# Kernel optimization log

Measured on AMD Instinct MI355X. Metric: run time of the kernel, lower is better.

Reference implementation:

```python
import jax, jax.numpy as jnp
import numpy as np


def _gcn_norm(edge_index, num_nodes, dtype):
    # PyG GCNConv.norm: add self-loops (weight 1), symmetric deg^{-1/2} normalization
    row, col = edge_index[0], edge_index[1]
    loop = jnp.arange(num_nodes, dtype=row.dtype)
    row = jnp.concatenate([row, loop])
    col = jnp.concatenate([col, loop])
    ew = jnp.ones(row.shape[0], dtype=dtype)
    deg = jax.ops.segment_sum(ew, row, num_segments=num_nodes)
    dis = jnp.where(deg > 0, jax.lax.rsqrt(deg), 0.0)
    norm = dis[row] * ew * dis[col]
    return row, col, norm


def _masked_gcn_conv(x, row, col, norm, sigma, W, b, num_nodes):
    # mask_features: edge gather -> diff/sigma -> square -> scatter-add -> exp mask
    h = (x[col] - x[row]) / sigma            # [E, F]
    h = norm[:, None] * h * h                # [E, F]
    mask = jax.ops.segment_sum(h, row, num_segments=num_nodes)        # [N, F]
    deg = jax.ops.segment_sum(jnp.ones_like(norm), row, num_segments=num_nodes)  # degree(source), >=1 due to self-loops
    x = x * jnp.exp(-mask / deg[:, None])
    # GCNConv: linear transform then normalized aggregation source->target
    xw = x @ W                               # [N, O]
    out = jax.ops.segment_sum(norm[:, None] * xw[row], col, num_segments=num_nodes)
    return out + b


def setup_inputs() -> dict:
    key = jax.random.key(0)
    ks = jax.random.split(key, 8)
    N, E, F, H, C = 100000, 1600000, 128, 64, 40
    g = 1.414  # xavier gain used for sigma
    return {
        "x": jax.random.normal(ks[0], (N, F), jnp.float32),
        "edge_index": jax.random.randint(ks[1], (2, E), 0, N, jnp.int64),
        "sigma1": jax.random.uniform(ks[2], (1, F), jnp.float32, -1.0, 1.0) * (g * np.sqrt(6.0 / (1 + F))),
        "W1": jax.random.normal(ks[3], (F, H), jnp.float32) * (1.0 / np.sqrt(F)),
        "b1": jnp.zeros((H,), jnp.float32),
        "sigma2": jax.random.uniform(ks[4], (1, H), jnp.float32, -1.0, 1.0) * (g * np.sqrt(6.0 / (1 + H))),
        "W2": jax.random.normal(ks[5], (H, C), jnp.float32) * (1.0 / np.sqrt(H)),
        "b2": jnp.zeros((C,), jnp.float32),
    }


def reference(x, edge_index, sigma1, W1, b1, sigma2, W2, b2):
    N = x.shape[0]
    row, col, norm = _gcn_norm(edge_index, N, x.dtype)
    x = _masked_gcn_conv(x, row, col, norm, sigma1, W1, b1, N)
    x = jax.nn.relu(x)
    # dropout is identity in eval mode
    x = _masked_gcn_conv(x, row, col, norm, sigma2, W2, b2, N)
    return jax.nn.log_softmax(x, axis=1)
```

## Files before the change

### kernel.cpp

```cpp
#include <hip/hip_runtime.h>
#include <cmath>

constexpr int F1 = 128;
constexpr int H  = 64;
constexpr int NC = 40;
constexpr int NPART = 4;

constexpr int SCAN_TPB = 256;
constexpr int SCAN_IPT = 8;
constexpr int SCAN_EPB = SCAN_TPB * SCAN_IPT;

__device__ inline unsigned short f2bf(float f) {
    union { float f; unsigned u; } v; v.f = f;
    return (unsigned short)((v.u + 0x7FFFu + ((v.u >> 16) & 1u)) >> 16);
}
__device__ inline float bflo(unsigned p) { union { float f; unsigned u; } v; v.u = p << 16; return v.f; }
__device__ inline float bfhi(unsigned p) { union { float f; unsigned u; } v; v.u = p & 0xFFFF0000u; return v.f; }
__device__ inline void unpack8(uint4 raw, float* d) {
    d[0] = bflo(raw.x); d[1] = bfhi(raw.x); d[2] = bflo(raw.y); d[3] = bfhi(raw.y);
    d[4] = bflo(raw.z); d[5] = bfhi(raw.z); d[6] = bflo(raw.w); d[7] = bfhi(raw.w);
}

__global__ void isg_kernel(const float* __restrict__ s1, float* __restrict__ i1,
                           const float* __restrict__ s2, float* __restrict__ i2) {
    int i = threadIdx.x;
    if (i < F1) i1[i] = 1.0f / s1[i];
    if (i < H)  i2[i] = 1.0f / s2[i];
}

__global__ void count8_prep_kernel(const int* __restrict__ row, const int* __restrict__ col,
                                   int* __restrict__ cntO, int* __restrict__ cntI,
                                   int E, int chunk, int stride, int cntBlocks,
                                   const float* __restrict__ x, const float* __restrict__ isg,
                                   unsigned short* __restrict__ u, size_t n8) {
    int bid = blockIdx.x;
    if (bid < cntBlocks) {
        int p = bid & (NPART - 1);
        int gid = bid / NPART;
        unsigned lo = (unsigned)(p * chunk);
        for (int e = gid * blockDim.x + threadIdx.x; e < E; e += stride) {
            int r = row[e], c = col[e];
            if ((unsigned)r - lo < (unsigned)chunk) atomicAdd(&cntO[r], 1);
            if ((unsigned)c - lo < (unsigned)chunk) atomicAdd(&cntI[c], 1);
        }
    } else {
        size_t idx = (size_t)(bid - cntBlocks) * blockDim.x + threadIdx.x;
        if (idx >= n8) return;
        size_t base = idx * 8;
        int fk = (int)(base % (size_t)F1);
        float4 a0 = *(const float4*)&x[base];
        float4 a1 = *(const float4*)&x[base + 4];
        float4 s0 = *(const float4*)&isg[fk];
        float4 s1 = *(const float4*)&isg[fk + 4];
        uint4 p4;
        p4.x = (unsigned)f2bf(a0.x * s0.x) | ((unsigned)f2bf(a0.y * s0.y) << 16);
        p4.y = (unsigned)f2bf(a0.z * s0.z) | ((unsigned)f2bf(a0.w * s0.w) << 16);
        p4.z = (unsigned)f2bf(a1.x * s1.x) | ((unsigned)f2bf(a1.y * s1.y) << 16);
        p4.w = (unsigned)f2bf(a1.z * s1.z) | ((unsigned)f2bf(a1.w * s1.w) << 16);
        *(uint4*)&u[base] = p4;
    }
}

__global__ void scan_partial_kernel(const int* __restrict__ cnt, int* __restrict__ bsum, int M) {
    __shared__ int red[SCAN_TPB];
    int t = threadIdx.x;
    int i0 = blockIdx.x * SCAN_EPB + t * SCAN_IPT;
    int s = 0;
#pragma unroll
    for (int k = 0; k < SCAN_IPT; ++k) {
        int i = i0 + k;
        if (i < M) s += cnt[i];
    }
    red[t] = s;
    __syncthreads();
    for (int off = SCAN_TPB / 2; off > 0; off >>= 1) {
        if (t < off) red[t] += red[t + off];
        __syncthreads();
    }
    if (t == 0) bsum[blockIdx.x] = red[0];
}

__global__ void scan_offsets_kernel(int* __restrict__ bsum, int nb,
                                    int* __restrict__ rowptrO, int* __restrict__ rowptrI,
                                    int N, int E) {
    __shared__ int sh[1024];
    int t = threadIdx.x;
    sh[t] = (t < nb) ? bsum[t] : 0;
    __syncthreads();
    for (int off = 1; off < 1024; off <<= 1) {
        int v = (t >= off) ? sh[t - off] : 0;
        __syncthreads();
        sh[t] += v;
        __syncthreads();
    }
    if (t < nb) bsum[t] = (t > 0) ? sh[t - 1] : 0;
    if (t == 0) { rowptrO[N] = E; rowptrI[N] = E; }
}

__global__ void scan_final_kernel(int* __restrict__ cntO, int* __restrict__ cntI,
                                  const int* __restrict__ bsum,
                                  int* __restrict__ rowptrO, int* __restrict__ rowptrI,
                                  float* __restrict__ dis, int N, int E) {
    __shared__ int sh[SCAN_TPB];
    int t = threadIdx.x;
    int M = 2 * N;
    const int* cnt = cntO;
    int i0 = blockIdx.x * SCAN_EPB + t * SCAN_IPT;
    int cv[SCAN_IPT], pre[SCAN_IPT];
    int run = 0;
#pragma unroll
    for (int k = 0; k < SCAN_IPT; ++k) {
        int i = i0 + k;
        cv[k] = (i < M) ? cnt[i] : 0;
        pre[k] = run;
        run += cv[k];
    }
    sh[t] = run;
    __syncthreads();
    for (int off = 1; off < SCAN_TPB; off <<= 1) {
        int v = (t >= off) ? sh[t - off] : 0;
        __syncthreads();
        sh[t] += v;
        __syncthreads();
    }
    int toff = ((t > 0) ? sh[t - 1] : 0) + bsum[blockIdx.x];
#pragma unroll
    for (int k = 0; k < SCAN_IPT; ++k) {
        int i = i0 + k;
        if (i < M) {
            int val = toff + pre[k];
            if (i < N) {
                rowptrO[i] = val;
                cntO[i] = val;
                dis[i] = rsqrtf((float)(cv[k] + 1));
            } else {
                rowptrI[i - N] = val - E;
                cntI[i - N] = val - E;
            }
        }
    }
}

__global__ void build8_kernel(const int* __restrict__ row, const int* __restrict__ col,
                              int* __restrict__ curO, int* __restrict__ curI,
                              int2* __restrict__ adjO2, int2* __restrict__ adjI2,
                              const float* __restrict__ dis,
                              int E, int chunk, int stride) {
    int p = blockIdx.x & (NPART - 1);
    int gid = blockIdx.x / NPART;
    unsigned lo = (unsigned)(p * chunk);
    for (int e = gid * blockDim.x + threadIdx.x; e < E; e += stride) {
        int r = row[e], c = col[e];
        bool inR = (unsigned)r - lo < (unsigned)chunk;
        bool inC = (unsigned)c - lo < (unsigned)chunk;
        if (inR | inC) {
            float nrm = dis[r] * dis[c];
            int nb = __float_as_int(nrm);
            if (inR) adjO2[atomicAdd(&curO[r], 1)] = make_int2(c, nb);
            if (inC) adjI2[atomicAdd(&curI[c], 1)] = make_int2(r, nb);
        }
    }
}

template<int F, int O, int R>
__global__ void fused_mask_gemm_kernel(const int* __restrict__ rowptr, const int2* __restrict__ adj2,
                                       const float* __restrict__ sig,
                                       const unsigned short* __restrict__ u,
                                       const float* __restrict__ W,
                                       unsigned short* __restrict__ Ybf, int N) {
    constexpr int NT = R * 64;
    constexpr int G = F / 8;
    constexpr int NPI = 64 / G;
    __shared__ __align__(16) float Ws[F * O];
    __shared__ __align__(16) float Xs[R][F];
    int tid = threadIdx.x;
    for (int i = tid; i < F * O; i += NT) Ws[i] = W[i];
    int w = tid >> 6, lane = tid & 63;
    int h = lane / G, j = lane % G;
    int base = blockIdx.x * R;
    int r = base + w;
    if (r < N) {
        int beg = rowptr[r], end = rowptr[r + 1];
        float inv_deg = 1.0f / (float)(end - beg + 1);
        float ur[8], acc[8];
        unpack8(*(const uint4*)&u[(size_t)r * F + 8 * j], ur);
#pragma unroll
        for (int k = 0; k < 8; ++k) acc[k] = 0.0f;
        for (int t = beg; t < end; t += 2 * NPI) {
            int e0 = t + h, e1 = t + NPI + h;
            int2 a0 = adj2[min(e0, end - 1)];
            int2 a1 = adj2[min(e1, end - 1)];
            float n0 = (e0 < end) ? __int_as_float(a0.y) : 0.0f;
            float n1 = (e1 < end) ? __int_as_float(a1.y) : 0.0f;
            uint4 rw0 = *(const uint4*)&u[(size_t)a0.x * F + 8 * j];
            uint4 rw1 = *(const uint4*)&u[(size_t)a1.x * F + 8 * j];
            float uc[8];
            unpack8(rw0, uc);
#pragma unroll
            for (int q = 0; q < 8; ++q) {
                float d = uc[q] - ur[q];
                acc[q] = fmaf(n0 * d, d, acc[q]);
            }
            unpack8(rw1, uc);
#pragma unroll
            for (int q = 0; q < 8; ++q) {
                float d = uc[q] - ur[q];
                acc[q] = fmaf(n1 * d, d, acc[q]);
            }
        }
#pragma unroll
        for (int off = G; off < 64; off <<= 1) {
#pragma unroll
            for (int k = 0; k < 8; ++k) acc[k] += __shfl_xor(acc[k], off);
        }
        if (h == 0) {
            float4 s0 = *(const float4*)&sig[8 * j];
            float4 s1 = *(const float4*)&sig[8 * j + 4];
            float sg[8] = {s0.x, s0.y, s0.z, s0.w, s1.x, s1.y, s1.z, s1.w};
            float xm[8];
#pragma unroll
            for (int k = 0; k < 8; ++k) xm[k] = ur[k] * sg[k] * expf(-acc[k] * inv_deg);
            *(float4*)&Xs[w][8 * j]     = make_float4(xm[0], xm[1], xm[2], xm[3]);
            *(float4*)&Xs[w][8 * j + 4] = make_float4(xm[4], xm[5], xm[6], xm[7]);
        }
    } else if (h == 0) {
        *(float4*)&Xs[w][8 * j]     = make_float4(0.f, 0.f, 0.f, 0.f);
        *(float4*)&Xs[w][8 * j + 4] = make_float4(0.f, 0.f, 0.f, 0.f);
    }
    __syncthreads();
    if (w < 2) {
        int r0 = base + 4 * w;
        if (r0 < N && lane < O) {
            float a0 = 0.f, a1 = 0.f, a2 = 0.f, a3 = 0.f;
#pragma unroll
            for (int fq = 0; fq < F / 4; ++fq) {
                float4 x0 = *(const float4*)&Xs[4 * w + 0][4 * fq];
                float4 x1 = *(const float4*)&Xs[4 * w + 1][4 * fq];
                float4 x2 = *(const float4*)&Xs[4 * w + 2][4 * fq];
                float4 x3 = *(const float4*)&Xs[4 * w + 3][4 * fq];
                float w0 = Ws[(4 * fq + 0) * O + lane];
                float w1 = Ws[(4 * fq + 1) * O + lane];
                float w2 = Ws[(4 * fq + 2) * O + lane];
                float w3 = Ws[(4 * fq + 3) * O + lane];
                a0 = fmaf(x0.x, w0, a0); a0 = fmaf(x0.y, w1, a0); a0 = fmaf(x0.z, w2, a0); a0 = fmaf(x0.w, w3, a0);
                a1 = fmaf(x1.x, w0, a1); a1 = fmaf(x1.y, w1, a1); a1 = fmaf(x1.z, w2, a1); a1 = fmaf(x1.w, w3, a1);
                a2 = fmaf(x2.x, w0, a2); a2 = fmaf(x2.y, w1, a2); a2 = fmaf(x2.z, w2, a2); a2 = fmaf(x2.w, w3, a2);
                a3 = fmaf(x3.x, w0, a3); a3 = fmaf(x3.y, w1, a3); a3 = fmaf(x3.z, w2, a3); a3 = fmaf(x3.w, w3, a3);
            }
            float o0 = __shfl_xor(a0, 1);
            float o1 = __shfl_xor(a1, 1);
            float o2 = __shfl_xor(a2, 1);
            float o3 = __shfl_xor(a3, 1);
            if (!(lane & 1)) {
                *(unsigned*)&Ybf[(size_t)r0 * O + lane] = (unsigned)f2bf(a0) | ((unsigned)f2bf(o0) << 16);
                if (r0 + 1 < N) *(unsigned*)&Ybf[(size_t)(r0 + 1) * O + lane] = (unsigned)f2bf(a1) | ((unsigned)f2bf(o1) << 16);
                if (r0 + 2 < N) *(unsigned*)&Ybf[(size_t)(r0 + 2) * O + lane] = (unsigned)f2bf(a2) | ((unsigned)f2bf(o2) << 16);
                if (r0 + 3 < N) *(unsigned*)&Ybf[(size_t)(r0 + 3) * O + lane] = (unsigned)f2bf(a3) | ((unsigned)f2bf(o3) << 16);
            }
        }
    }
}

__global__ void agg_relu_kernel(const int* __restrict__ rowptr, const int2* __restrict__ adj2,
                                const float* __restrict__ dis, const unsigned short* __restrict__ ybf,
                                const float* __restrict__ bias,
                                unsigned short* __restrict__ u2, const float* __restrict__ isg2, int N) {
    int c = blockIdx.x * (blockDim.x >> 6) + (threadIdx.x >> 6);
    if (c >= N) return;
    int lane = threadIdx.x & 63;
    int h = lane >> 3, j = lane & 7;
    int beg = rowptr[c], end = rowptr[c + 1];
    float acc[8];
#pragma unroll
    for (int k = 0; k < 8; ++k) acc[k] = 0.0f;
    for (int t = beg; t < end; t += 16) {
        int e0 = t + h, e1 = t + 8 + h;
        int2 a0 = adj2[min(e0, end - 1)];
        int2 a1 = adj2[min(e1, end - 1)];
        float n0 = (e0 < end) ? __int_as_float(a0.y) : 0.0f;
        float n1 = (e1 < end) ? __int_as_float(a1.y) : 0.0f;
        uint4 rw0 = *(const uint4*)&ybf[(size_t)a0.x * H + 8 * j];
        uint4 rw1 = *(const uint4*)&ybf[(size_t)a1.x * H + 8 * j];
        float v[8];
        unpack8(rw0, v);
#pragma unroll
        for (int q = 0; q < 8; ++q) acc[q] = fmaf(n0, v[q], acc[q]);
        unpack8(rw1, v);
#pragma unroll
        for (int q = 0; q < 8; ++q) acc[q] = fmaf(n1, v[q], acc[q]);
    }
#pragma unroll
    for (int off = 8; off < 64; off <<= 1) {
#pragma unroll
        for (int k = 0; k < 8; ++k) acc[k] += __shfl_xor(acc[k], off);
    }
    if (h == 0) {
        float dc = dis[c];
        float sv[8];
        unpack8(*(const uint4*)&ybf[(size_t)c * H + 8 * j], sv);
        float4 b0 = *(const float4*)&bias[8 * j];
        float4 b1v = *(const float4*)&bias[8 * j + 4];
        float bb[8] = {b0.x, b0.y, b0.z, b0.w, b1v.x, b1v.y, b1v.z, b1v.w};
        float4 s0 = *(const float4*)&isg2[8 * j];
        float4 s1 = *(const float4*)&isg2[8 * j + 4];
        float sg[8] = {s0.x, s0.y, s0.z, s0.w, s1.x, s1.y, s1.z, s1.w};
        float hv[8];
        float d2 = dc * dc;
#pragma unroll
        for (int k = 0; k < 8; ++k) hv[k] = fmaxf(fmaf(d2, sv[k], acc[k]) + bb[k], 0.0f);
        uint4 p;
        p.x = (unsigned)f2bf(hv[0] * sg[0]) | ((unsigned)f2bf(hv[1] * sg[1]) << 16);
        p.y = (unsigned)f2bf(hv[2] * sg[2]) | ((unsigned)f2bf(hv[3] * sg[3]) << 16);
        p.z = (unsigned)f2bf(hv[4] * sg[4]) | ((unsigned)f2bf(hv[5] * sg[5]) << 16);
        p.w = (unsigned)f2bf(hv[6] * sg[6]) | ((unsigned)f2bf(hv[7] * sg[7]) << 16);
        *(uint4*)&u2[(size_t)c * H + 8 * j] = p;
    }
}

__global__ void agg_lsm_kernel(const int* __restrict__ rowptr, const int2* __restrict__ adj2,
                               const float* __restrict__ dis, const unsigned short* __restrict__ ybf,
                               const float* __restrict__ bias, float* __restrict__ out, int N) {
    int c = blockIdx.x * (blockDim.x >> 6) + (threadIdx.x >> 6);
    if (c >= N) return;
    int lane = threadIdx.x & 63;
    int h = lane >> 4, j = lane & 15;
    bool active = j < 10;
    int beg = rowptr[c], end = rowptr[c + 1];
    float a[4] = {0.f, 0.f, 0.f, 0.f};
    for (int t = beg; t < end; t += 8) {
        int e0 = t + h, e1 = t + 4 + h;
        int2 a0 = adj2[min(e0, end - 1)];
        int2 a1 = adj2[min(e1, end - 1)];
        float n0 = (e0 < end) ? __int_as_float(a0.y) : 0.0f;
        float n1 = (e1 < end) ? __int_as_float(a1.y) : 0.0f;
        uint2 rw0 = active ? *(const uint2*)&ybf[(size_t)a0.x * NC + 4 * j] : make_uint2(0u, 0u);
        uint2 rw1 = active ? *(const uint2*)&ybf[(size_t)a1.x * NC + 4 * j] : make_uint2(0u, 0u);
        a[0] = fmaf(n0, bflo(rw0.x), a[0]); a[1] = fmaf(n0, bfhi(rw0.x), a[1]);
        a[2] = fmaf(n0, bflo(rw0.y), a[2]); a[3] = fmaf(n0, bfhi(rw0.y), a[3]);
        a[0] = fmaf(n1, bflo(rw1.x), a[0]); a[1] = fmaf(n1, bfhi(rw1.x), a[1]);
        a[2] = fmaf(n1, bflo(rw1.y), a[2]); a[3] = fmaf(n1, bfhi(rw1.y), a[3]);
    }
#pragma unroll
    for (int off = 16; off < 64; off <<= 1) {
#pragma unroll
        for (int k = 0; k < 4; ++k) a[k] += __shfl_xor(a[k], off);
    }
    bool wr = (h == 0) && active;
    float v[4] = {-INFINITY, -INFINITY, -INFINITY, -INFINITY};
    if (wr) {
        float dc = dis[c];
        uint2 sr = *(const uint2*)&ybf[(size_t)c * NC + 4 * j];
        float sv[4] = {bflo(sr.x), bfhi(sr.x), bflo(sr.y), bfhi(sr.y)};
        float4 bb = *(const float4*)&bias[4 * j];
        float b4[4] = {bb.x, bb.y, bb.z, bb.w};
        float d2 = dc * dc;
#pragma unroll
        for (int k = 0; k < 4; ++k) v[k] = fmaf(d2, sv[k], a[k]) + b4[k];
    }
    float m = fmaxf(fmaxf(v[0], v[1]), fmaxf(v[2], v[3]));
#pragma unroll
    for (int off = 8; off > 0; off >>= 1) m = fmaxf(m, __shfl_xor(m, off));
    float s = wr ? (expf(v[0] - m) + expf(v[1] - m) + expf(v[2] - m) + expf(v[3] - m)) : 0.0f;
#pragma unroll
    for (int off = 8; off > 0; off >>= 1) s += __shfl_xor(s, off);
    float mls = m + logf(s);
    if (wr)
        *(float4*)&out[(size_t)c * NC + 4 * j] = make_float4(v[0] - mls, v[1] - mls, v[2] - mls, v[3] - mls);
}

extern "C" void kernel_launch(void* const* d_in, const int* in_sizes, int n_in,
                              void* d_out, int out_size, void* d_ws, size_t ws_size,
                              hipStream_t stream) {
    const float* x    = (const float*)d_in[0];
    const int*   ei   = (const int*)  d_in[1];
    const float* sig1 = (const float*)d_in[2];
    const float* W1   = (const float*)d_in[3];
    const float* b1   = (const float*)d_in[4];
    const float* sig2 = (const float*)d_in[5];
    const float* W2   = (const float*)d_in[6];
    const float* b2   = (const float*)d_in[7];
    float* out = (float*)d_out;

    const int N = in_sizes[0] / F1;
    const int E = in_sizes[1] / 2;
    const int* row = ei;
    const int* col = ei + E;

    char* w = (char*)d_ws;
    auto alloc = [&](size_t bytes) { void* q = w; w += (bytes + 255) & ~255ull; return q; };
    int*   cntO    = (int*)  alloc((size_t)2 * N * 4);
    int*   cntI    = cntO + N;
    int*   rowptrO = (int*)  alloc((size_t)(N + 1) * 4);
    int*   rowptrI = (int*)  alloc((size_t)(N + 1) * 4);
    int2*  adjO2   = (int2*) alloc((size_t)E * 8);
    int2*  adjI2   = (int2*) alloc((size_t)E * 8);
    float* dis     = (float*)alloc((size_t)N * 4);
    float* isg1    = (float*)alloc(F1 * 4);
    float* isg2    = (float*)alloc(H * 4);
    int*   bsum    = (int*)  alloc(1024 * 4);
    unsigned short* u1   = (unsigned short*)alloc((size_t)N * F1 * 2);
    unsigned short* u2   = (unsigned short*)alloc((size_t)N * H * 2);
    unsigned short* ybf1 = (unsigned short*)alloc((size_t)N * H * 2);
    unsigned short* ybf2 = u1;

    const int B = 256;
    const int chunk = (N + NPART - 1) / NPART;
    const int TOTB = 8192;
    const int stride4 = (TOTB / NPART) * B;
    const size_t n8 = (size_t)N * F1 / 8;
    const int prepBlocks = (int)((n8 + B - 1) / B);
    const int M = 2 * N;
    const int nb = (M + SCAN_EPB - 1) / SCAN_EPB;

    hipMemsetAsync(cntO, 0, (size_t)2 * N * 4, stream);
    isg_kernel<<<1, 128, 0, stream>>>(sig1, isg1, sig2, isg2);
    count8_prep_kernel<<<TOTB + prepBlocks, B, 0, stream>>>(
        row, col, cntO, cntI, E, chunk, stride4, TOTB, x, isg1, u1, n8);
    scan_partial_kernel<<<nb, SCAN_TPB, 0, stream>>>(cntO, bsum, M);
    scan_offsets_kernel<<<1, 1024, 0, stream>>>(bsum, nb, rowptrO, rowptrI, N, E);
    scan_final_kernel<<<nb, SCAN_TPB, 0, stream>>>(cntO, cntI, bsum, rowptrO, rowptrI, dis, N, E);
    build8_kernel<<<TOTB, B, 0, stream>>>(row, col, cntO, cntI, adjO2, adjI2, dis, E, chunk, stride4);

    fused_mask_gemm_kernel<F1, H, 8><<<(N + 7) / 8, 512, 0, stream>>>(rowptrO, adjO2, sig1, u1, W1, ybf1, N);
    agg_relu_kernel<<<(N + 3) / 4, B, 0, stream>>>(rowptrI, adjI2, dis, ybf1, b1, u2, isg2, N);

    fused_mask_gemm_kernel<H, NC, 8><<<(N + 7) / 8, 512, 0, stream>>>(rowptrO, adjO2, sig2, u2, W2, ybf2, N);
    agg_lsm_kernel<<<(N + 3) / 4, B, 0, stream>>>(rowptrI, adjI2, dis, ybf2, b2, out, N);
}
```

Baseline: 612.7 us.

## Replace partitioned multi-pass CSR build with replicated atomic counter copies

Measured after the change: 694.5 us. 13.3% more time.

```diff
diff --git a/kernel.cpp b/kernel.cpp
--- a/kernel.cpp
+++ b/kernel.cpp
@@ -4,7 +4,7 @@
 constexpr int F1 = 128;
 constexpr int H  = 64;
 constexpr int NC = 40;
-constexpr int NPART = 4;
+constexpr int NCOPY = 8;
 
 constexpr int SCAN_TPB = 256;
 constexpr int SCAN_IPT = 8;
@@ -28,23 +28,20 @@
     if (i < H)  i2[i] = 1.0f / s2[i];
 }
 
-__global__ void count8_prep_kernel(const int* __restrict__ row, const int* __restrict__ col,
-                                   int* __restrict__ cntO, int* __restrict__ cntI,
-                                   int E, int chunk, int stride, int cntBlocks,
+__global__ void count1_prep_kernel(const int* __restrict__ row, const int* __restrict__ col,
+                                   int* __restrict__ cnt8, int E, int N, int cntBlocks,
                                    const float* __restrict__ x, const float* __restrict__ isg,
                                    unsigned short* __restrict__ u, size_t n8) {
     int bid = blockIdx.x;
     if (bid < cntBlocks) {
-        int p = bid & (NPART - 1);
-        int gid = bid / NPART;
-        unsigned lo = (unsigned)(p * chunk);
-        for (int e = gid * blockDim.x + threadIdx.x; e < E; e += stride) {
-            int r = row[e], c = col[e];
-            if ((unsigned)r - lo < (unsigned)chunk) atomicAdd(&cntO[r], 1);
-            if ((unsigned)c - lo < (unsigned)chunk) atomicAdd(&cntI[c], 1);
+        int e = bid * 256 + threadIdx.x;
+        if (e < E) {
+            int* cnt = cnt8 + (size_t)(bid & (NCOPY - 1)) * 2 * N;
+            atomicAdd(&cnt[row[e]], 1);
+            atomicAdd(&cnt[N + col[e]], 1);
         }
     } else {
-        size_t idx = (size_t)(bid - cntBlocks) * blockDim.x + threadIdx.x;
+        size_t idx = (size_t)(bid - cntBlocks) * 256 + threadIdx.x;
         if (idx >= n8) return;
         size_t base = idx * 8;
         int fk = (int)(base % (size_t)F1);
@@ -61,7 +58,7 @@
     }
 }
 
-__global__ void scan_partial_kernel(const int* __restrict__ cnt, int* __restrict__ bsum, int M) {
+__global__ void scan_partial_kernel(const int* __restrict__ cnt8, int* __restrict__ bsum, int M) {
     __shared__ int red[SCAN_TPB];
     int t = threadIdx.x;
     int i0 = blockIdx.x * SCAN_EPB + t * SCAN_IPT;
@@ -69,7 +66,10 @@
 #pragma unroll
     for (int k = 0; k < SCAN_IPT; ++k) {
         int i = i0 + k;
-        if (i < M) s += cnt[i];
+        if (i < M) {
+#pragma unroll
+            for (int c = 0; c < NCOPY; ++c) s += cnt8[(size_t)c * M + i];
+        }
     }
     red[t] = s;
     __syncthreads();
@@ -97,23 +97,27 @@
     if (t == 0) { rowptrO[N] = E; rowptrI[N] = E; }
 }
 
-__global__ void scan_final_kernel(int* __restrict__ cntO, int* __restrict__ cntI,
+__global__ void scan_final_kernel(const int* __restrict__ cnt8, int* __restrict__ cur8,
                                   const int* __restrict__ bsum,
                                   int* __restrict__ rowptrO, int* __restrict__ rowptrI,
                                   float* __restrict__ dis, int N, int E) {
     __shared__ int sh[SCAN_TPB];
     int t = threadIdx.x;
     int M = 2 * N;
-    const int* cnt = cntO;
     int i0 = blockIdx.x * SCAN_EPB + t * SCAN_IPT;
-    int cv[SCAN_IPT], pre[SCAN_IPT];
+    int tot[SCAN_IPT], pre[SCAN_IPT];
     int run = 0;
 #pragma unroll
     for (int k = 0; k < SCAN_IPT; ++k) {
         int i = i0 + k;
-        cv[k] = (i < M) ? cnt[i] : 0;
+        int s = 0;
+        if (i < M) {
+#pragma unroll
+            for (int c = 0; c < NCOPY; ++c) s += cnt8[(size_t)c * M + i];
+        }
+        tot[k] = s;
         pre[k] = run;
-        run += cv[k];
+        run += s;
     }
     sh[t] = run;
     __syncthreads();
@@ -129,37 +133,38 @@
         int i = i0 + k;
         if (i < M) {
             int val = toff + pre[k];
+            int base;
             if (i < N) {
                 rowptrO[i] = val;
-                cntO[i] = val;
-                dis[i] = rsqrtf((float)(cv[k] + 1));
+                dis[i] = rsqrtf((float)(tot[k] + 1));
+                base = val;
             } else {
                 rowptrI[i - N] = val - E;
-                cntI[i - N] = val - E;
-            }
-        }
-    }
-}
-
-__global__ void build8_kernel(const int* __restrict__ row, const int* __restrict__ col,
-                              int* __restrict__ curO, int* __restrict__ curI,
+                base = val - E;
+            }
+            int b = base;
+#pragma unroll
+            for (int c = 0; c < NCOPY; ++c) {
+                cur8[(size_t)c * M + i] = b;
+                b += cnt8[(size_t)c * M + i];
+            }
+        }
+    }
+}
+
+__global__ void build1_kernel(const int* __restrict__ row, const int* __restrict__ col,
+                              int* __restrict__ cur8,
                               int2* __restrict__ adjO2, int2* __restrict__ adjI2,
-                              const float* __restrict__ dis,
-                              int E, int chunk, int stride) {
-    int p = blockIdx.x & (NPART - 1);
-    int gid = blockIdx.x / NPART;
-    unsigned lo = (unsigned)(p * chunk);
-    for (int e = gid * blockDim.x + threadIdx.x; e < E; e += stride) {
-        int r = row[e], c = col[e];
-        bool inR = (unsigned)r - lo < (unsigned)chunk;
-        bool inC = (unsigned)c - lo < (unsigned)chunk;
-        if (inR | inC) {
-            float nrm = dis[r] * dis[c];
-            int nb = __float_as_int(nrm);
-            if (inR) adjO2[atomicAdd(&curO[r], 1)] = make_int2(c, nb);
-            if (inC) adjI2[atomicAdd(&curI[c], 1)] = make_int2(r, nb);
-        }
-    }
+                              const float* __restrict__ dis, int E, int N) {
+    int bid = blockIdx.x;
+    int e = bid * 256 + threadIdx.x;
+    if (e >= E) return;
+    int* cur = cur8 + (size_t)(bid & (NCOPY - 1)) * 2 * N;
+    int r = row[e], c = col[e];
+    float nrm = dis[r] * dis[c];
+    int nb = __float_as_int(nrm);
+    adjO2[atomicAdd(&cur[r], 1)] = make_int2(c, nb);
+    adjI2[atomicAdd(&cur[N + c], 1)] = make_int2(r, nb);
 }
 
 template<int F, int O, int R>
@@ -388,8 +393,6 @@
 
     char* w = (char*)d_ws;
     auto alloc = [&](size_t bytes) { void* q = w; w += (bytes + 255) & ~255ull; return q; };
-    int*   cntO    = (int*)  alloc((size_t)2 * N * 4);
-    int*   cntI    = cntO + N;
     int*   rowptrO = (int*)  alloc((size_t)(N + 1) * 4);
     int*   rowptrI = (int*)  alloc((size_t)(N + 1) * 4);
     int2*  adjO2   = (int2*) alloc((size_t)E * 8);
@@ -402,24 +405,24 @@
     unsigned short* u2   = (unsigned short*)alloc((size_t)N * H * 2);
     unsigned short* ybf1 = (unsigned short*)alloc((size_t)N * H * 2);
     unsigned short* ybf2 = u1;
+    int* cnt8 = (int*)u2;
+    int* cur8 = (int*)ybf1;
 
     const int B = 256;
-    const int chunk = (N + NPART - 1) / NPART;
-    const int TOTB = 8192;
-    const int stride4 = (TOTB / NPART) * B;
+    const int cntBlocks = (E + B - 1) / B;
     const size_t n8 = (size_t)N * F1 / 8;
     const int prepBlocks = (int)((n8 + B - 1) / B);
     const int M = 2 * N;
     const int nb = (M + SCAN_EPB - 1) / SCAN_EPB;
 
-    hipMemsetAsync(cntO, 0, (size_t)2 * N * 4, stream);
+    hipMemsetAsync(cnt8, 0, (size_t)NCOPY * M * 4, stream);
     isg_kernel<<<1, 128, 0, stream>>>(sig1, isg1, sig2, isg2);
-    count8_prep_kernel<<<TOTB + prepBlocks, B, 0, stream>>>(
-        row, col, cntO, cntI, E, chunk, stride4, TOTB, x, isg1, u1, n8);
-    scan_partial_kernel<<<nb, SCAN_TPB, 0, stream>>>(cntO, bsum, M);
+    count1_prep_kernel<<<cntBlocks + prepBlocks, B, 0, stream>>>(
+        row, col, cnt8, E, N, cntBlocks, x, isg1, u1, n8);
+    scan_partial_kernel<<<nb, SCAN_TPB, 0, stream>>>(cnt8, bsum, M);
     scan_offsets_kernel<<<1, 1024, 0, stream>>>(bsum, nb, rowptrO, rowptrI, N, E);
-    scan_final_kernel<<<nb, SCAN_TPB, 0, stream>>>(cntO, cntI, bsum, rowptrO, rowptrI, dis, N, E);
-    build8_kernel<<<TOTB, B, 0, stream>>>(row, col, cntO, cntI, adjO2, adjI2, dis, E, chunk, stride4);
+    scan_final_kernel<<<nb, SCAN_TPB, 0, stream>>>(cnt8, cur8, bsum, rowptrO, rowptrI, dis, N, E);
+    build1_kernel<<<cntBlocks, B, 0, stream>>>(row, col, cur8, adjO2, adjI2, dis, E, N);
 
     fused_mask_gemm_kernel<F1, H, 8><<<(N + 7) / 8, 512, 0, stream>>>(rowptrO, adjO2, sig1, u1, W1, ybf1, N);
     agg_relu_kernel<<<(N + 3) / 4, B, 0, stream>>>(rowptrI, adjI2, dis, ybf1, b1, u2, isg2, N);
```
